# Kernel optimization log

Measured on AMD Instinct MI355X. Metric: run time of the kernel, lower is better.

The kernel has to match this reference:

```python
import jax, jax.numpy as jnp
import numpy as np

N_NODES = 65536
N_EDGES = 1048576
VOCAB = 50000
HIDDEN = 256
LAYERS = 3
NUM_GRAPHS = 64
NEG_SLOPE = 0.2  # PyG GATConv default LeakyReLU slope
EPS = 1e-16      # PyG softmax denominator epsilon


def setup_inputs() -> dict:
    key = jax.random.key(0)
    ks = jax.random.split(key, 12)
    s = 0.02
    nodes = jax.random.randint(ks[0], (N_NODES,), 0, VOCAB, dtype=jnp.int32)
    edge_index = jax.random.randint(ks[1], (2, N_EDGES), 0, N_NODES, dtype=jnp.int32)
    batch = jnp.sort(jax.random.randint(ks[2], (N_NODES,), 0, NUM_GRAPHS, dtype=jnp.int32))
    emb = jax.random.normal(ks[3], (VOCAB, HIDDEN), jnp.float32) * s
    Wg = jax.random.normal(ks[4], (LAYERS, HIDDEN, HIDDEN), jnp.float32) * s
    a_src = jax.random.normal(ks[5], (LAYERS, HIDDEN), jnp.float32) * s
    a_dst = jax.random.normal(ks[6], (LAYERS, HIDDEN), jnp.float32) * s
    bg = jnp.zeros((LAYERS, HIDDEN), jnp.float32)
    Wl = jax.random.normal(ks[7], (LAYERS, HIDDEN, HIDDEN), jnp.float32) * s
    bl = jnp.zeros((LAYERS, HIDDEN), jnp.float32)
    Wout = jax.random.normal(ks[8], (HIDDEN, VOCAB), jnp.float32) * s
    bout = jnp.zeros((VOCAB,), jnp.float32)
    return {"nodes": nodes, "edge_index": edge_index, "batch": batch,
            "emb": emb, "Wg": Wg, "a_src": a_src, "a_dst": a_dst, "bg": bg,
            "Wl": Wl, "bl": bl, "Wout": Wout, "bout": bout}


def _gat_layer(x, src, dst, W, a_s, a_d, b, n):
    h = x @ W                                    # [N, H]
    e = jax.nn.leaky_relu((h @ a_s)[src] + (h @ a_d)[dst], NEG_SLOPE)  # [E]
    m = jax.ops.segment_max(e, dst, num_segments=n)
    w = jnp.exp(e - m[dst])
    denom = jax.ops.segment_sum(w, dst, num_segments=n)
    alpha = w / (denom[dst] + EPS)               # segment softmax over incoming edges
    out = jax.ops.segment_sum(h[src] * alpha[:, None], dst, num_segments=n)
    return out + b


def reference(nodes, edge_index, batch, emb, Wg, a_src, a_dst, bg, Wl, bl, Wout, bout):
    n = nodes.shape[0]
    loop = jnp.arange(n, dtype=edge_index.dtype)  # GATConv add_self_loops=True
    src = jnp.concatenate([edge_index[0], loop])
    dst = jnp.concatenate([edge_index[1], loop])
    x = emb[nodes]                                # [N, H]
    for l in range(Wg.shape[0]):
        x = _gat_layer(x, src, dst, Wg[l], a_src[l], a_dst[l], bg[l], n)
        x = jax.nn.relu(x)
        x = x @ Wl[l] + bl[l]
    sums = jax.ops.segment_sum(x, batch, num_segments=NUM_GRAPHS)
    cnt = jax.ops.segment_sum(jnp.ones((n,), x.dtype), batch, num_segments=NUM_GRAPHS)
    pooled = sums / jnp.maximum(cnt, 1.0)[:, None]  # global mean pool -> [G, H]
    return pooled @ Wout + bout                      # [G, V]
```

## Files before the change

kernel.cpp:

```cpp
#include <hip/hip_runtime.h>

#define N_NODES 65536
#define N_EDGES 1048576
#define E_TOTAL (N_EDGES + N_NODES)
#define VOCAB 50000
#define HIDDEN 256
#define NUM_GRAPHS 64
#define NEG_SLOPE 0.2f
#define SM_EPS 1e-16f

#define NBKT 128
#define BKT_SHIFT 9
#define DSTS_PER_BKT 512
#define BKT_CAP 10240
#define EDGES_PER_BLK1 4352

typedef _Float16 f16x8 __attribute__((ext_vector_type(8)));
typedef _Float16 f16x4 __attribute__((ext_vector_type(4)));
typedef float f32x4 __attribute__((ext_vector_type(4)));

__global__ __launch_bounds__(256) void gather_kernel(const int* __restrict__ nodes,
    const float* __restrict__ emb, _Float16* __restrict__ x) {
    int i = blockIdx.x;
    int t = threadIdx.x;
    x[(size_t)i * HIDDEN + t] = (_Float16)emb[(size_t)nodes[i] * HIDDEN + t];
}

__global__ __launch_bounds__(256) void convert_wt_kernel(const float* __restrict__ Wg,
    const float* __restrict__ Wl, _Float16* __restrict__ WT) {
    int mat = blockIdx.y;
    int n = blockIdx.x;
    int k = threadIdx.x;
    const float* W = (mat < 3) ? (Wg + (size_t)mat * HIDDEN * HIDDEN)
                               : (Wl + (size_t)(mat - 3) * HIDDEN * HIDDEN);
    WT[(size_t)mat * HIDDEN * HIDDEN + (size_t)n * HIDDEN + k] = (_Float16)W[(size_t)k * HIDDEN + n];
}


__global__ __launch_bounds__(256) void bucket_kernel(const int* __restrict__ ei,
    int* __restrict__ bcur, unsigned* __restrict__ staging) {
    __shared__ int lhist[NBKT];
    __shared__ int lbase[NBKT];
    __shared__ int lcur[NBKT];
    int tid = threadIdx.x;
    if (tid < NBKT) lhist[tid] = 0;
    __syncthreads();
    int e0 = blockIdx.x * EDGES_PER_BLK1;
    int mySrc[17], myDst[17];
    #pragma unroll
    for (int k = 0; k < 17; k++) {
        int e = e0 + k * 256 + tid;
        int src, dst;
        if (e < N_EDGES) { src = ei[e]; dst = ei[N_EDGES + e]; }
        else             { src = dst = e - N_EDGES; }
        mySrc[k] = src; myDst[k] = dst;
        atomicAdd(&lhist[dst >> BKT_SHIFT], 1);
    }
    __syncthreads();
    if (tid < NBKT) {
        int c = lhist[tid];
        lbase[tid] = (c > 0) ? atomicAdd(&bcur[tid], c) : 0;
        lcur[tid] = 0;
    }
    __syncthreads();
    #pragma unroll
    for (int k = 0; k < 17; k++) {
        int b = myDst[k] >> BKT_SHIFT;
        int pos = lbase[b] + atomicAdd(&lcur[b], 1);
        staging[(size_t)b * BKT_CAP + pos] =
            ((unsigned)(myDst[k] & (DSTS_PER_BKT - 1)) << 16) | (unsigned)mySrc[k];
    }
}

__global__ __launch_bounds__(256) void csr_kernel(const int* __restrict__ bcur,
    const unsigned* __restrict__ staging, int* __restrict__ row_ptr,
    int* __restrict__ src_sorted) {
    __shared__ unsigned sedge[BKT_CAP];
    __shared__ int shist[DSTS_PER_BKT];
    __shared__ int sbase[DSTS_PER_BKT];
    __shared__ int spart[256];
    int b = blockIdx.x;
    int tid = threadIdx.x;
    int cnt = bcur[b];

    spart[tid] = (tid < NBKT && tid < b) ? bcur[tid] : 0;
    __syncthreads();
    for (int d = 128; d > 0; d >>= 1) {
        if (tid < d) spart[tid] += spart[tid + d];
        __syncthreads();
    }
    int base = spart[0];
    __syncthreads();

    shist[tid] = 0; shist[tid + 256] = 0;
    __syncthreads();
    for (int i = tid; i < cnt; i += 256) {
        unsigned v = staging[(size_t)b * BKT_CAP + i];
        sedge[i] = v;
        atomicAdd(&shist[v >> 16], 1);
    }
    __syncthreads();
    int p = shist[2 * tid] + shist[2 * tid + 1];
    spart[tid] = p;
    __syncthreads();
    for (int d = 1; d < 256; d <<= 1) {
        int v = (tid >= d) ? spart[tid - d] : 0;
        __syncthreads();
        spart[tid] += v;
        __syncthreads();
    }
    int epair = spart[tid] - p;
    sbase[2 * tid] = epair;
    sbase[2 * tid + 1] = epair + shist[2 * tid];
    __syncthreads();
    row_ptr[b * DSTS_PER_BKT + tid] = base + sbase[tid];
    row_ptr[b * DSTS_PER_BKT + 256 + tid] = base + sbase[256 + tid];
    shist[tid] = sbase[tid];
    shist[tid + 256] = sbase[tid + 256];
    __syncthreads();
    for (int i = tid; i < cnt; i += 256) {
        unsigned v = sedge[i];
        int d = v >> 16;
        int pos = atomicAdd(&shist[d], 1);
        src_sorted[base + pos] = (int)(v & 0xFFFFu);
    }
    if (b == NBKT - 1 && tid == 0) row_ptr[N_NODES] = E_TOTAL;
}

#define PAD_K 40
template <bool FUSED>
__global__ __launch_bounds__(256) void gemm_f16_kernel(const _Float16* __restrict__ A,
    const _Float16* __restrict__ WT, const float* __restrict__ bias,
    _Float16* __restrict__ C,
    const float* __restrict__ a_s, const float* __restrict__ a_d,
    float* __restrict__ es, float* __restrict__ ed) {
    __shared__ _Float16 As[128][PAD_K];
    __shared__ _Float16 Bs[128][PAD_K];
    int tid = threadIdx.x;
    int wave = tid >> 6;
    int lane = tid & 63;
    int quad = lane >> 4;
    int l16 = lane & 15;
    int m0 = blockIdx.x * 128;
    int n0 = blockIdx.y * 128;

    f32x4 acc[2][8];
    #pragma unroll
    for (int rt = 0; rt < 2; rt++)
        #pragma unroll
        for (int ct = 0; ct < 8; ct++)
            acc[rt][ct] = (f32x4){0.f, 0.f, 0.f, 0.f};

    for (int k0 = 0; k0 < HIDDEN; k0 += 32) {
        __syncthreads();
        #pragma unroll
        for (int i = 0; i < 2; i++) {
            int c = tid + i * 256;
            int row = c >> 2, q = c & 3;
            *(f16x8*)&As[row][q * 8] =
                *(const f16x8*)(A + (size_t)(m0 + row) * HIDDEN + k0 + q * 8);
        }
        #pragma unroll
        for (int i = 0; i < 2; i++) {
            int c = tid + i * 256;
            int row = c >> 2, q = c & 3;
            *(f16x8*)&Bs[row][q * 8] =
                *(const f16x8*)(WT + (size_t)(n0 + row) * HIDDEN + k0 + q * 8);
        }
        __syncthreads();
        f16x8 a0 = *(const f16x8*)&As[wave * 32 + l16][quad * 8];
        f16x8 a1 = *(const f16x8*)&As[wave * 32 + 16 + l16][quad * 8];
        #pragma unroll
        for (int ct = 0; ct < 8; ct++) {
            f16x8 b = *(const f16x8*)&Bs[ct * 16 + l16][quad * 8];
            acc[0][ct] = __builtin_amdgcn_mfma_f32_16x16x32_f16(a0, b, acc[0][ct], 0, 0, 0);
            acc[1][ct] = __builtin_amdgcn_mfma_f32_16x16x32_f16(a1, b, acc[1][ct], 0, 0, 0);
        }
    }
    #pragma unroll
    for (int rt = 0; rt < 2; rt++) {
        #pragma unroll
        for (int ct = 0; ct < 8; ct++) {
            int col = n0 + ct * 16 + l16;
            float bv = (bias != nullptr) ? bias[col] : 0.f;
            int rowbase = m0 + wave * 32 + rt * 16 + quad * 4;
            #pragma unroll
            for (int r = 0; r < 4; r++) {
                C[(size_t)(rowbase + r) * HIDDEN + col] = (_Float16)(acc[rt][ct][r] + bv);
            }
        }
    }
    if (FUSED) {
        #pragma unroll
        for (int rt = 0; rt < 2; rt++) {
            float ds0 = 0.f, ds1 = 0.f, ds2 = 0.f, ds3 = 0.f;
            float dd0 = 0.f, dd1 = 0.f, dd2 = 0.f, dd3 = 0.f;
            #pragma unroll
            for (int ct = 0; ct < 8; ct++) {
                int col = n0 + ct * 16 + l16;
                float av = a_s[col];
                float dv = a_d[col];
                ds0 += acc[rt][ct][0] * av; dd0 += acc[rt][ct][0] * dv;
                ds1 += acc[rt][ct][1] * av; dd1 += acc[rt][ct][1] * dv;
                ds2 += acc[rt][ct][2] * av; dd2 += acc[rt][ct][2] * dv;
                ds3 += acc[rt][ct][3] * av; dd3 += acc[rt][ct][3] * dv;
            }
            #pragma unroll
            for (int off = 1; off < 16; off <<= 1) {
                ds0 += __shfl_xor(ds0, off); dd0 += __shfl_xor(dd0, off);
                ds1 += __shfl_xor(ds1, off); dd1 += __shfl_xor(dd1, off);
                ds2 += __shfl_xor(ds2, off); dd2 += __shfl_xor(dd2, off);
                ds3 += __shfl_xor(ds3, off); dd3 += __shfl_xor(dd3, off);
            }
            if (l16 == 0) {
                int rowbase = m0 + wave * 32 + rt * 16 + quad * 4;
                atomicAdd(&es[rowbase + 0], ds0); atomicAdd(&ed[rowbase + 0], dd0);
                atomicAdd(&es[rowbase + 1], ds1); atomicAdd(&ed[rowbase + 1], dd1);
                atomicAdd(&es[rowbase + 2], ds2); atomicAdd(&ed[rowbase + 2], dd2);
                atomicAdd(&es[rowbase + 3], ds3); atomicAdd(&ed[rowbase + 3], dd3);
            }
        }
    }
}

__global__ __launch_bounds__(256) void agg_kernel(const _Float16* __restrict__ h,
    const int* __restrict__ row_ptr, const int* __restrict__ src_sorted,
    const float* __restrict__ es, const float* __restrict__ ed,
    const float* __restrict__ bg, _Float16* __restrict__ g) {
    int dst = blockIdx.x * 8 + (threadIdx.x >> 5);
    int l32 = threadIdx.x & 31;
    int start = row_ptr[dst];
    int end = row_ptr[dst + 1];
    float edd = ed[dst];
    const _Float16* hl = h + l32 * 8;

    float den0 = 0.f, den1 = 0.f;
    float acc[8];
    #pragma unroll
    for (int j = 0; j < 8; j++) acc[j] = 0.f;

    int i = start;
    for (; i + 7 < end; i += 8) {
        int s0 = src_sorted[i + 0];
        int s1 = src_sorted[i + 1];
        int s2 = src_sorted[i + 2];
        int s3 = src_sorted[i + 3];
        int s4 = src_sorted[i + 4];
        int s5 = src_sorted[i + 5];
        int s6 = src_sorted[i + 6];
        int s7 = src_sorted[i + 7];
        f16x8 r0 = *(const f16x8*)(hl + (unsigned)s0 * HIDDEN);
        f16x8 r1 = *(const f16x8*)(hl + (unsigned)s1 * HIDDEN);
        f16x8 r2 = *(const f16x8*)(hl + (unsigned)s2 * HIDDEN);
        f16x8 r3 = *(const f16x8*)(hl + (unsigned)s3 * HIDDEN);
        f16x8 r4 = *(const f16x8*)(hl + (unsigned)s4 * HIDDEN);
        f16x8 r5 = *(const f16x8*)(hl + (unsigned)s5 * HIDDEN);
        f16x8 r6 = *(const f16x8*)(hl + (unsigned)s6 * HIDDEN);
        f16x8 r7 = *(const f16x8*)(hl + (unsigned)s7 * HIDDEN);
        float e0 = es[s0] + edd; e0 = (e0 > 0.f) ? e0 : NEG_SLOPE * e0;
        float e1 = es[s1] + edd; e1 = (e1 > 0.f) ? e1 : NEG_SLOPE * e1;
        float e2 = es[s2] + edd; e2 = (e2 > 0.f) ? e2 : NEG_SLOPE * e2;
        float e3 = es[s3] + edd; e3 = (e3 > 0.f) ? e3 : NEG_SLOPE * e3;
        float e4 = es[s4] + edd; e4 = (e4 > 0.f) ? e4 : NEG_SLOPE * e4;
        float e5 = es[s5] + edd; e5 = (e5 > 0.f) ? e5 : NEG_SLOPE * e5;
        float e6 = es[s6] + edd; e6 = (e6 > 0.f) ? e6 : NEG_SLOPE * e6;
        float e7 = es[s7] + edd; e7 = (e7 > 0.f) ? e7 : NEG_SLOPE * e7;
        float w0 = __expf(e0);
        float w1 = __expf(e1);
        float w2 = __expf(e2);
        float w3 = __expf(e3);
        float w4 = __expf(e4);
        float w5 = __expf(e5);
        float w6 = __expf(e6);
        float w7 = __expf(e7);
        den0 += (w0 + w1) + (w2 + w3);
        den1 += (w4 + w5) + (w6 + w7);
        #pragma unroll
        for (int j = 0; j < 8; j++)
            acc[j] += (w0 * (float)r0[j] + w1 * (float)r1[j])
                    + (w2 * (float)r2[j] + w3 * (float)r3[j])
                    + (w4 * (float)r4[j] + w5 * (float)r5[j])
                    + (w6 * (float)r6[j] + w7 * (float)r7[j]);
    }
    for (; i + 3 < end; i += 4) {
        int s0 = src_sorted[i + 0];
        int s1 = src_sorted[i + 1];
        int s2 = src_sorted[i + 2];
        int s3 = src_sorted[i + 3];
        f16x8 r0 = *(const f16x8*)(hl + (unsigned)s0 * HIDDEN);
        f16x8 r1 = *(const f16x8*)(hl + (unsigned)s1 * HIDDEN);
        f16x8 r2 = *(const f16x8*)(hl + (unsigned)s2 * HIDDEN);
        f16x8 r3 = *(const f16x8*)(hl + (unsigned)s3 * HIDDEN);
        float e0 = es[s0] + edd; e0 = (e0 > 0.f) ? e0 : NEG_SLOPE * e0;
        float e1 = es[s1] + edd; e1 = (e1 > 0.f) ? e1 : NEG_SLOPE * e1;
        float e2 = es[s2] + edd; e2 = (e2 > 0.f) ? e2 : NEG_SLOPE * e2;
        float e3 = es[s3] + edd; e3 = (e3 > 0.f) ? e3 : NEG_SLOPE * e3;
        float w0 = __expf(e0);
        float w1 = __expf(e1);
        float w2 = __expf(e2);
        float w3 = __expf(e3);
        den0 += (w0 + w1) + (w2 + w3);
        #pragma unroll
        for (int j = 0; j < 8; j++)
            acc[j] += (w0 * (float)r0[j] + w1 * (float)r1[j])
                    + (w2 * (float)r2[j] + w3 * (float)r3[j]);
    }
    for (; i < end; i++) {
        int s0 = src_sorted[i];
        f16x8 r0 = *(const f16x8*)(hl + (unsigned)s0 * HIDDEN);
        float e0 = es[s0] + edd; e0 = (e0 > 0.f) ? e0 : NEG_SLOPE * e0;
        float w0 = __expf(e0);
        den1 += w0;
        #pragma unroll
        for (int j = 0; j < 8; j++) acc[j] += w0 * (float)r0[j];
    }

    float inv = 1.0f / ((den0 + den1) + SM_EPS);
    float4 b0 = *(const float4*)(bg + l32 * 8);
    float4 b1 = *(const float4*)(bg + l32 * 8 + 4);
    f16x8 outv;
    outv[0] = (_Float16)fmaxf(acc[0] * inv + b0.x, 0.f);
    outv[1] = (_Float16)fmaxf(acc[1] * inv + b0.y, 0.f);
    outv[2] = (_Float16)fmaxf(acc[2] * inv + b0.z, 0.f);
    outv[3] = (_Float16)fmaxf(acc[3] * inv + b0.w, 0.f);
    outv[4] = (_Float16)fmaxf(acc[4] * inv + b1.x, 0.f);
    outv[5] = (_Float16)fmaxf(acc[5] * inv + b1.y, 0.f);
    outv[6] = (_Float16)fmaxf(acc[6] * inv + b1.z, 0.f);
    outv[7] = (_Float16)fmaxf(acc[7] * inv + b1.w, 0.f);
    *(f16x8*)(g + (size_t)dst * HIDDEN + l32 * 8) = outv;
}

__global__ __launch_bounds__(128) void graph_bounds_kernel(const int* __restrict__ batch,
    int* __restrict__ gstart) {
    int g = threadIdx.x;
    if (g > NUM_GRAPHS) return;
    if (g == NUM_GRAPHS) { gstart[NUM_GRAPHS] = N_NODES; return; }
    int lo = 0, hi = N_NODES;
    while (lo < hi) {
        int mid = (lo + hi) >> 1;
        if (batch[mid] < g) lo = mid + 1; else hi = mid;
    }
    gstart[g] = lo;
}

#define POOL_SPLITS 16
__global__ __launch_bounds__(256) void pool_partial_kernel(const _Float16* __restrict__ x,
    const int* __restrict__ gstart, float* __restrict__ pooledT) {
    int g = blockIdx.x;
    int chunk = blockIdx.y;
    int t = threadIdx.x;
    int s = gstart[g];
    int e = gstart[g + 1];
    int n = e - s;
    int per = (n + POOL_SPLITS - 1) / POOL_SPLITS;
    int r0 = s + chunk * per;
    int r1 = min(r0 + per, e);
    if (r0 >= r1) return;
    float acc = 0.f;
    for (int r = r0; r < r1; r++) acc += (float)x[(size_t)r * HIDDEN + t];
    atomicAdd(&pooledT[t * NUM_GRAPHS + g], acc);
}

__global__ __launch_bounds__(256) void mean_kernel(const float* __restrict__ pooledT,
    const int* __restrict__ gstart, float* __restrict__ meanT) {
    int i = blockIdx.x * 256 + threadIdx.x;
    int g = i & (NUM_GRAPHS - 1);
    float c = (float)max(gstart[g + 1] - gstart[g], 1);
    meanT[i] = pooledT[i] / c;
}

__global__ __launch_bounds__(256) void final_kernel(const float* __restrict__ meanT,
    const float* __restrict__ Wout, const float* __restrict__ bout, float* __restrict__ out) {
    int j = blockIdx.x * 64 + (threadIdx.x & 63);
    int g0 = __builtin_amdgcn_readfirstlane((threadIdx.x >> 6) * 16);
    if (j >= VOCAB) return;
    float acc[16];
    #pragma unroll
    for (int g = 0; g < 16; g++) acc[g] = 0.f;
    #pragma unroll 4
    for (int k = 0; k < HIDDEN; k++) {
        float w = Wout[(size_t)k * VOCAB + j];
        const float* mrow = meanT + k * NUM_GRAPHS + g0;
        #pragma unroll
        for (int g = 0; g < 16; g++) acc[g] += mrow[g] * w;
    }
    float b = bout[j];
    #pragma unroll
    for (int g = 0; g < 16; g++) out[(size_t)(g0 + g) * VOCAB + j] = acc[g] + b;
}

extern "C" void kernel_launch(void* const* d_in, const int* in_sizes, int n_in,
                              void* d_out, int out_size, void* d_ws, size_t ws_size,
                              hipStream_t stream) {
    const int*   nodes = (const int*)d_in[0];
    const int*   ei    = (const int*)d_in[1];
    const int*   batch = (const int*)d_in[2];
    const float* emb   = (const float*)d_in[3];
    const float* Wg    = (const float*)d_in[4];
    const float* a_src = (const float*)d_in[5];
    const float* a_dst = (const float*)d_in[6];
    const float* bg    = (const float*)d_in[7];
    const float* Wl    = (const float*)d_in[8];
    const float* bl    = (const float*)d_in[9];
    const float* Wout  = (const float*)d_in[10];
    const float* bout  = (const float*)d_in[11];
    float* out = (float*)d_out;

    char* ws = (char*)d_ws;
    size_t off = 0;
    auto alloc = [&](size_t bytes) -> void* {
        void* p = ws + off;
        off += (bytes + 255) & ~(size_t)255;
        return p;
    };
    _Float16* bufA    = (_Float16*)alloc((size_t)N_NODES * HIDDEN * 2);
    _Float16* bufB    = (_Float16*)alloc((size_t)N_NODES * HIDDEN * 2);
    _Float16* WT      = (_Float16*)alloc((size_t)6 * HIDDEN * HIDDEN * 2);
    float* es         = (float*)alloc((size_t)N_NODES * 4);
    float* ed         = (float*)alloc((size_t)N_NODES * 4);
    int*   row_ptr    = (int*)alloc((size_t)(N_NODES + 1) * 4);
    int*   src_sorted = (int*)alloc((size_t)E_TOTAL * 4);
    int*   bcur       = (int*)alloc((size_t)NBKT * 4);
    unsigned* staging = (unsigned*)alloc((size_t)NBKT * BKT_CAP * 4);
    float* pooledT    = (float*)alloc((size_t)HIDDEN * NUM_GRAPHS * 4);
    float* meanT      = (float*)alloc((size_t)HIDDEN * NUM_GRAPHS * 4);
    int*   gstart     = (int*)alloc((size_t)(NUM_GRAPHS + 1) * 4);

    hipMemsetAsync(bcur, 0, (size_t)NBKT * 4, stream);
    hipMemsetAsync(pooledT, 0, (size_t)HIDDEN * NUM_GRAPHS * 4, stream);

    convert_wt_kernel<<<dim3(HIDDEN, 6), 256, 0, stream>>>(Wg, Wl, WT);
    gather_kernel<<<N_NODES, 256, 0, stream>>>(nodes, emb, bufA);
    bucket_kernel<<<E_TOTAL / EDGES_PER_BLK1, 256, 0, stream>>>(ei, bcur, staging);
    csr_kernel<<<NBKT, 256, 0, stream>>>(bcur, staging, row_ptr, src_sorted);

    _Float16* cur = bufA;
    _Float16* oth = bufB;
    for (int l = 0; l < 3; l++) {
        hipMemsetAsync(es, 0, (size_t)N_NODES * 4, stream);
        hipMemsetAsync(ed, 0, (size_t)N_NODES * 4, stream);
        gemm_f16_kernel<true><<<dim3(N_NODES / 128, 2), 256, 0, stream>>>(
            cur, WT + (size_t)l * HIDDEN * HIDDEN, nullptr, oth,
            a_src + (size_t)l * HIDDEN, a_dst + (size_t)l * HIDDEN, es, ed);
        agg_kernel<<<N_NODES / 8, 256, 0, stream>>>(
            oth, row_ptr, src_sorted, es, ed, bg + (size_t)l * HIDDEN, cur);
        gemm_f16_kernel<false><<<dim3(N_NODES / 128, 2), 256, 0, stream>>>(
            cur, WT + (size_t)(3 + l) * HIDDEN * HIDDEN, bl + (size_t)l * HIDDEN, oth,
            nullptr, nullptr, nullptr, nullptr);
        _Float16* t = cur; cur = oth; oth = t;
    }

    graph_bounds_kernel<<<1, 128, 0, stream>>>(batch, gstart);
    pool_partial_kernel<<<dim3(NUM_GRAPHS, POOL_SPLITS), 256, 0, stream>>>(cur, gstart, pooledT);
    mean_kernel<<<(HIDDEN * NUM_GRAPHS) / 256, 256, 0, stream>>>(pooledT, gstart, meanT);
    final_kernel<<<dim3((VOCAB + 63) / 64), 256, 0, stream>>>(meanT, Wout, bout, out);
}
```

Measured before the change: 718.5 us.

## Fold post-ReLU linear layers into next GAT weights and defer last past pooling

The per-node Wl linear of layers 0 and 1 is folded algebraically into the next layer's Wg, using fused weights Wl·Wg and bias bl·Wg computed on device. The last layer's Wl is applied after mean pooling on the 64x256 pooled matrix, which is valid because the map is affine and the pool is a mean. The fused GEMM epilogue now adds the bias into the accumulator before computing the attention dot products. This drops three full N×256×256 GEMMs and their fp16 round trips, at the cost of small weight-prep kernels and a different fp16 rounding path.

```diff
diff --git a/kernel.cpp b/kernel.cpp
--- a/kernel.cpp
+++ b/kernel.cpp
@@ -27,15 +27,34 @@
 }
 
 __global__ __launch_bounds__(256) void convert_wt_kernel(const float* __restrict__ Wg,
-    const float* __restrict__ Wl, _Float16* __restrict__ WT) {
-    int mat = blockIdx.y;
+    _Float16* __restrict__ WT) {
     int n = blockIdx.x;
     int k = threadIdx.x;
-    const float* W = (mat < 3) ? (Wg + (size_t)mat * HIDDEN * HIDDEN)
-                               : (Wl + (size_t)(mat - 3) * HIDDEN * HIDDEN);
-    WT[(size_t)mat * HIDDEN * HIDDEN + (size_t)n * HIDDEN + k] = (_Float16)W[(size_t)k * HIDDEN + n];
-}
-
+    WT[(size_t)n * HIDDEN + k] = (_Float16)Wg[(size_t)k * HIDDEN + n];
+}
+
+__global__ __launch_bounds__(256) void fuse_w_kernel(const float* __restrict__ Wl,
+    const float* __restrict__ Wg, _Float16* __restrict__ WT) {
+    int pair = blockIdx.y;
+    int n = blockIdx.x;
+    int k = threadIdx.x;
+    const float* A = Wl + (size_t)pair * HIDDEN * HIDDEN;
+    const float* B = Wg + (size_t)(pair + 1) * HIDDEN * HIDDEN;
+    float s = 0.f;
+    for (int j = 0; j < HIDDEN; j++) s += A[(size_t)k * HIDDEN + j] * B[(size_t)j * HIDDEN + n];
+    WT[(size_t)(1 + pair) * HIDDEN * HIDDEN + (size_t)n * HIDDEN + k] = (_Float16)s;
+}
+
+__global__ __launch_bounds__(256) void fuse_b_kernel(const float* __restrict__ Wg,
+    const float* __restrict__ bl, float* __restrict__ bfused) {
+    int pair = blockIdx.x;
+    int n = threadIdx.x;
+    const float* B = Wg + (size_t)(pair + 1) * HIDDEN * HIDDEN;
+    const float* b = bl + (size_t)pair * HIDDEN;
+    float s = 0.f;
+    for (int k = 0; k < HIDDEN; k++) s += b[k] * B[(size_t)k * HIDDEN + n];
+    bfused[pair * HIDDEN + n] = s;
+}
 
 __global__ __launch_bounds__(256) void bucket_kernel(const int* __restrict__ ei,
     int* __restrict__ bcur, unsigned* __restrict__ staging) {
@@ -186,7 +205,9 @@
             int rowbase = m0 + wave * 32 + rt * 16 + quad * 4;
             #pragma unroll
             for (int r = 0; r < 4; r++) {
-                C[(size_t)(rowbase + r) * HIDDEN + col] = (_Float16)(acc[rt][ct][r] + bv);
+                float hv = acc[rt][ct][r] + bv;
+                acc[rt][ct][r] = hv;
+                C[(size_t)(rowbase + r) * HIDDEN + col] = (_Float16)hv;
             }
         }
     }
@@ -369,6 +390,18 @@
     meanT[i] = pooledT[i] / c;
 }
 
+__global__ __launch_bounds__(256) void wl2_kernel(const float* __restrict__ meanP,
+    const float* __restrict__ Wl, const float* __restrict__ bl,
+    float* __restrict__ meanT2) {
+    int g = blockIdx.x;
+    int n = threadIdx.x;
+    const float* W2 = Wl + (size_t)2 * HIDDEN * HIDDEN;
+    float s = bl[2 * HIDDEN + n];
+    for (int k = 0; k < HIDDEN; k++)
+        s += meanP[k * NUM_GRAPHS + g] * W2[(size_t)k * HIDDEN + n];
+    meanT2[n * NUM_GRAPHS + g] = s;
+}
+
 __global__ __launch_bounds__(256) void final_kernel(const float* __restrict__ meanT,
     const float* __restrict__ Wout, const float* __restrict__ bout, float* __restrict__ out) {
     int j = blockIdx.x * 64 + (threadIdx.x & 63);
@@ -415,7 +448,8 @@
     };
     _Float16* bufA    = (_Float16*)alloc((size_t)N_NODES * HIDDEN * 2);
     _Float16* bufB    = (_Float16*)alloc((size_t)N_NODES * HIDDEN * 2);
-    _Float16* WT      = (_Float16*)alloc((size_t)6 * HIDDEN * HIDDEN * 2);
+    _Float16* WT      = (_Float16*)alloc((size_t)3 * HIDDEN * HIDDEN * 2);
+    float* bfused     = (float*)alloc((size_t)2 * HIDDEN * 4);
     float* es         = (float*)alloc((size_t)N_NODES * 4);
     float* ed         = (float*)alloc((size_t)N_NODES * 4);
     int*   row_ptr    = (int*)alloc((size_t)(N_NODES + 1) * 4);
@@ -424,34 +458,33 @@
     unsigned* staging = (unsigned*)alloc((size_t)NBKT * BKT_CAP * 4);
     float* pooledT    = (float*)alloc((size_t)HIDDEN * NUM_GRAPHS * 4);
     float* meanT      = (float*)alloc((size_t)HIDDEN * NUM_GRAPHS * 4);
+    float* meanT2     = (float*)alloc((size_t)HIDDEN * NUM_GRAPHS * 4);
     int*   gstart     = (int*)alloc((size_t)(NUM_GRAPHS + 1) * 4);
 
     hipMemsetAsync(bcur, 0, (size_t)NBKT * 4, stream);
     hipMemsetAsync(pooledT, 0, (size_t)HIDDEN * NUM_GRAPHS * 4, stream);
 
-    convert_wt_kernel<<<dim3(HIDDEN, 6), 256, 0, stream>>>(Wg, Wl, WT);
+    convert_wt_kernel<<<HIDDEN, 256, 0, stream>>>(Wg, WT);
+    fuse_w_kernel<<<dim3(HIDDEN, 2), 256, 0, stream>>>(Wl, Wg, WT);
+    fuse_b_kernel<<<2, 256, 0, stream>>>(Wg, bl, bfused);
     gather_kernel<<<N_NODES, 256, 0, stream>>>(nodes, emb, bufA);
     bucket_kernel<<<E_TOTAL / EDGES_PER_BLK1, 256, 0, stream>>>(ei, bcur, staging);
     csr_kernel<<<NBKT, 256, 0, stream>>>(bcur, staging, row_ptr, src_sorted);
 
-    _Float16* cur = bufA;
-    _Float16* oth = bufB;
     for (int l = 0; l < 3; l++) {
         hipMemsetAsync(es, 0, (size_t)N_NODES * 4, stream);
         hipMemsetAsync(ed, 0, (size_t)N_NODES * 4, stream);
+        const float* bias = (l == 0) ? nullptr : (bfused + (size_t)(l - 1) * HIDDEN);
         gemm_f16_kernel<true><<<dim3(N_NODES / 128, 2), 256, 0, stream>>>(
-            cur, WT + (size_t)l * HIDDEN * HIDDEN, nullptr, oth,
+            bufA, WT + (size_t)l * HIDDEN * HIDDEN, bias, bufB,
             a_src + (size_t)l * HIDDEN, a_dst + (size_t)l * HIDDEN, es, ed);
         agg_kernel<<<N_NODES / 8, 256, 0, stream>>>(
-            oth, row_ptr, src_sorted, es, ed, bg + (size_t)l * HIDDEN, cur);
-        gemm_f16_kernel<false><<<dim3(N_NODES / 128, 2), 256, 0, stream>>>(
-            cur, WT + (size_t)(3 + l) * HIDDEN * HIDDEN, bl + (size_t)l * HIDDEN, oth,
-            nullptr, nullptr, nullptr, nullptr);
-        _Float16* t = cur; cur = oth; oth = t;
+            bufB, row_ptr, src_sorted, es, ed, bg + (size_t)l * HIDDEN, bufA);
     }
 
     graph_bounds_kernel<<<1, 128, 0, stream>>>(batch, gstart);
-    pool_partial_kernel<<<dim3(NUM_GRAPHS, POOL_SPLITS), 256, 0, stream>>>(cur, gstart, pooledT);
+    pool_partial_kernel<<<dim3(NUM_GRAPHS, POOL_SPLITS), 256, 0, stream>>>(bufA, gstart, pooledT);
     mean_kernel<<<(HIDDEN * NUM_GRAPHS) / 256, 256, 0, stream>>>(pooledT, gstart, meanT);
-    final_kernel<<<dim3((VOCAB + 63) / 64), 256, 0, stream>>>(meanT, Wout, bout, out);
-}
+    wl2_kernel<<<NUM_GRAPHS, 256, 0, stream>>>(meanT, Wl, bl, meanT2);
+    final_kernel<<<dim3((VOCAB + 63) / 64), 256, 0, stream>>>(meanT2, Wout, bout, out);
+}
```

Measured after the change: 694.1 us. 3.4% less time.
